# Kernel optimization log

Measured on AMD Instinct MI355X. Metric: run time of the kernel, lower is better.

Reference implementation:

```python
import jax, jax.numpy as jnp
import numpy as np

KS = 7  # transform conv kernel size


def setup_inputs() -> dict:
    key = jax.random.key(0)
    kx, kq, kk, kv, kt = jax.random.split(key, 5)
    b, c, h, w = 4, 64, 64, 64
    x = jax.random.normal(kx, (b, c, h, w), dtype=jnp.float32)
    # 1x1 convs (out_channel=1, bias=False) -> weight vectors over channels
    q_w = jax.random.normal(kq, (c,), dtype=jnp.float32) * 0.05
    k_w = jax.random.normal(kk, (c,), dtype=jnp.float32) * 0.05
    v_w = jax.random.normal(kv, (c,), dtype=jnp.float32) * 0.05
    # transform conv: 1 -> 1 channel, 7x7, reflect pad, no bias
    t_w = jax.random.normal(kt, (1, 1, KS, KS), dtype=jnp.float32) * 0.05
    return {"x": x, "q_w": q_w, "k_w": k_w, "v_w": v_w, "t_w": t_w}


def reference(x, q_w, k_w, v_w, t_w):
    b, c, h, w = x.shape
    hw = h * w
    # 1x1 convs to single channel, flattened over spatial dims -> [b, HW]
    q = jnp.einsum('bchw,c->bhw', x, q_w).reshape(b, hw)
    k = jnp.einsum('bchw,c->bhw', x, k_w).reshape(b, hw)
    v = jnp.einsum('bchw,c->bhw', x, v_w).reshape(b, hw)
    # degenerate head_dim=1 attention: scores are an outer product [b, HW, HW]
    scores = q[:, :, None] * k[:, None, :]
    attn_w = jax.nn.softmax(scores, axis=-1)
    attn = jnp.einsum('bij,bj->bi', attn_w, v).reshape(b, 1, h, w)
    # transform: reflect-pad then 7x7 valid conv
    pad = KS // 2
    attn_p = jnp.pad(attn, ((0, 0), (0, 0), (pad, pad), (pad, pad)), mode='reflect')
    out = jax.lax.conv_general_dilated(
        attn_p, t_w, window_strides=(1, 1), padding='VALID',
        dimension_numbers=('NCHW', 'OIHW', 'NCHW'))
    return out
```

## Files before the change

kernel.cpp:

```cpp
#include <hip/hip_runtime.h>

#define C 64
#define HW 4096
#define NM 20
#define SIG 0x7E3A91D4u
#define PSTRIDE 112
#define PBASE 4096

__device__ __constant__ float INVF[NM] = {
    1.0000000000e+00f, 1.0000000000e+00f, 5.0000000000e-01f, 1.6666666667e-01f,
    4.1666666667e-02f, 8.3333333333e-03f, 1.3888888889e-03f, 1.9841269841e-04f,
    2.4801587302e-05f, 2.7557319224e-06f, 2.7557319224e-07f, 2.5052108385e-08f,
    2.0876756988e-09f, 1.6059043837e-10f, 1.1470745598e-11f, 7.6471637318e-13f,
    4.7794773324e-14f, 2.8114572543e-15f, 1.5619206968e-16f, 8.2206352466e-18f
};

__device__ __forceinline__ void st_rlx(uint32_t* p, uint32_t v) {
    __hip_atomic_store(p, v, __ATOMIC_RELAXED, __HIP_MEMORY_SCOPE_AGENT);
}
__device__ __forceinline__ uint32_t ld_rlx(const uint32_t* p) {
    return __hip_atomic_load(p, __ATOMIC_RELAXED, __HIP_MEMORY_SCOPE_AGENT);
}
__device__ __forceinline__ int reflect64(int r) {
    return r < 0 ? -r : (r > 63 ? 126 - r : r);
}

__global__ __launch_bounds__(256) void fused_kernel(
    const float* __restrict__ x,
    const float* __restrict__ qw,
    const float* __restrict__ kw,
    const float* __restrict__ vw,
    const float* __restrict__ tw,
    float* __restrict__ out,
    uint32_t* __restrict__ W) {
    __shared__ float pq[4][64], pk[4][64], pv[4][64];
    __shared__ float kk[64], vv[64];
    __shared__ float red[64 * 41];
    __shared__ float wred[4][40];
    __shared__ float cf[2 * NM];
    __shared__ float q_lds[7][64];
    __shared__ float attn_s[7][64];
    __shared__ float wgt[49];

    const int tid = threadIdx.x;
    const int p = tid & 63;
    const int wv = tid >> 6;
    const int bl = blockIdx.x;
    const int b = bl >> 6, y = bl & 63;

    uint32_t* flags = W;
    uint32_t* part = W + PBASE + bl * PSTRIDE;

    const float* xb = x + ((size_t)b * C + wv * 16) * HW + y * 64 + p;
    float qa = 0.f, ka = 0.f, va = 0.f;
#pragma unroll
    for (int c = 0; c < 16; ++c) {
        float xv = xb[(size_t)c * HW];
        qa = fmaf(xv, qw[wv * 16 + c], qa);
        ka = fmaf(xv, kw[wv * 16 + c], ka);
        va = fmaf(xv, vw[wv * 16 + c], va);
    }
    pq[wv][p] = qa; pk[wv][p] = ka; pv[wv][p] = va;
    if (tid < 49) wgt[tid] = tw[tid];
    __syncthreads();

    if (wv == 0) {
        float qf = (pq[0][p] + pq[1][p]) + (pq[2][p] + pq[3][p]);
        float kf = (pk[0][p] + pk[1][p]) + (pk[2][p] + pk[3][p]);
        float vf = (pv[0][p] + pv[1][p]) + (pv[2][p] + pv[3][p]);
        st_rlx(part + 40 + p, __float_as_uint(qf));
        kk[p] = kf; vv[p] = vf; q_lds[3][p] = qf;
    }
    __syncthreads();

    {
        float k1 = kk[p], v1 = vv[p];
        float t = 1.f;
        if (wv != 0) {
            float k2 = k1 * k1, k4 = k2 * k2, k5 = k4 * k1;
            t = k5;
            if (wv == 2) t = k5 * k5;
            if (wv == 3) t = (k5 * k5) * k5;
        }
#pragma unroll
        for (int j = 0; j < 5; ++j) {
            red[p * 41 + 5 * wv + j] = t;
            red[p * 41 + 20 + 5 * wv + j] = t * v1;
            t *= k1;
        }
    }
    __syncthreads();

    if (p < 2 * NM) {
        float s = 0.f;
#pragma unroll
        for (int i = 0; i < 16; ++i) s += red[(wv * 16 + i) * 41 + p];
        wred[wv][p] = s;
    }
    __syncthreads();
    if (tid < 2 * NM) {
        float s = (wred[0][tid] + wred[1][tid]) + (wred[2][tid] + wred[3][tid]);
        s *= INVF[tid < NM ? tid : tid - NM];
        st_rlx(part + tid, __float_as_uint(s));
    }
    asm volatile("s_waitcnt vmcnt(0)" ::: "memory");
    __syncthreads();
    if (tid == 0) st_rlx(flags + bl, SIG);

    if (wv == 0) {
        const uint32_t* f = flags + b * 64 + p;
        bool done = false;
        int guard = 0;
        while (true) {
            if (!done) done = (ld_rlx(f) == SIG);
            if (__all(done)) break;
            if (++guard > (1 << 16)) break;
            __builtin_amdgcn_s_sleep(1);
        }
        asm volatile("" ::: "memory");
        if (p < 2 * NM) {
            uint32_t t[64];
            const uint32_t* pb = W + PBASE + (b * 64) * PSTRIDE + p;
#pragma unroll
            for (int s = 0; s < 64; ++s) t[s] = ld_rlx(pb + s * PSTRIDE);
            float fs[64];
#pragma unroll
            for (int s = 0; s < 64; ++s) fs[s] = __uint_as_float(t[s]);
#pragma unroll
            for (int st = 1; st < 64; st <<= 1)
#pragma unroll
                for (int i = 0; i < 64; i += 2 * st) fs[i] += fs[i + st];
            cf[p] = fs[0];
        }
    } else {
        int oA = (wv == 1) ? 0 : (wv == 2) ? 2 : 5;
        int oB = (wv == 1) ? 1 : (wv == 2) ? 4 : 6;
        int rA = reflect64(y + oA - 3);
        int rB = reflect64(y + oB - 3);
        bool needA = (rA != y), needB = (rB != y);
        const uint32_t* fA = flags + b * 64 + rA;
        const uint32_t* fB = flags + b * 64 + rB;
        int guard = 0;
        while (true) {
            bool ok = (!needA || ld_rlx(fA) == SIG) &&
                      (!needB || ld_rlx(fB) == SIG);
            if (ok) break;
            if (++guard > (1 << 16)) break;
            __builtin_amdgcn_s_sleep(1);
        }
        asm volatile("" ::: "memory");
        float hA = needA
            ? __uint_as_float(ld_rlx(W + PBASE + (b * 64 + rA) * PSTRIDE + 40 + p))
            : q_lds[3][p];
        float hB = needB
            ? __uint_as_float(ld_rlx(W + PBASE + (b * 64 + rB) * PSTRIDE + 40 + p))
            : q_lds[3][p];
        q_lds[oA][p] = hA;
        q_lds[oB][p] = hB;
    }
    __syncthreads();

#pragma unroll
    for (int pass = 0; pass < 2; ++pass) {
        int s = pass * 256 + tid;
        int o = s >> 6, cc = s & 63;
        if (o < 7) {
            float qv = q_lds[o][cc];
            float ng = cf[NM - 1], nf = cf[2 * NM - 1];
#pragma unroll
            for (int mm = NM - 2; mm >= 0; --mm) {
                ng = fmaf(ng, qv, cf[mm]);
                nf = fmaf(nf, qv, cf[NM + mm]);
            }
            attn_s[o][cc] = nf / ng;
        }
    }
    __syncthreads();

    if (wv == 0) {
        float acc = 0.f;
#pragma unroll
        for (int dy = 0; dy < 7; ++dy) {
#pragma unroll
            for (int dx = 0; dx < 7; ++dx) {
                int xx = p + dx - 3;
                xx = xx < 0 ? -xx : (xx > 63 ? 126 - xx : xx);
                acc = fmaf(attn_s[dy][xx], wgt[dy * 7 + dx], acc);
            }
        }
        out[(size_t)b * HW + y * 64 + p] = acc;
    }
}

extern "C" void kernel_launch(void* const* d_in, const int* in_sizes, int n_in,
                              void* d_out, int out_size, void* d_ws, size_t ws_size,
                              hipStream_t stream) {
    const float* x  = (const float*)d_in[0];
    const float* qw = (const float*)d_in[1];
    const float* kw = (const float*)d_in[2];
    const float* vw = (const float*)d_in[3];
    const float* tw = (const float*)d_in[4];
    float* out = (float*)d_out;
    uint32_t* W = (uint32_t*)d_ws;

    fused_kernel<<<256, 256, 0, stream>>>(x, qw, kw, vw, tw, out, W);
}
```

Before: 11.82 us.

## Split cross-block coefficient reduction and 7x7 conv across all four waves

```diff
diff --git a/kernel.cpp b/kernel.cpp
--- a/kernel.cpp
+++ b/kernel.cpp
@@ -37,9 +37,11 @@
     __shared__ float kk[64], vv[64];
     __shared__ float red[64 * 41];
     __shared__ float wred[4][40];
+    __shared__ float gred[4][40];
     __shared__ float cf[2 * NM];
     __shared__ float q_lds[7][64];
     __shared__ float attn_s[7][64];
+    __shared__ float cacc[4][64];
     __shared__ float wgt[49];
 
     const int tid = threadIdx.x;
@@ -104,10 +106,9 @@
         st_rlx(part + tid, __float_as_uint(s));
     }
     asm volatile("s_waitcnt vmcnt(0)" ::: "memory");
-    __syncthreads();
     if (tid == 0) st_rlx(flags + bl, SIG);
 
-    if (wv == 0) {
+    {
         const uint32_t* f = flags + b * 64 + p;
         bool done = false;
         int guard = 0;
@@ -118,45 +119,45 @@
             __builtin_amdgcn_s_sleep(1);
         }
         asm volatile("" ::: "memory");
-        if (p < 2 * NM) {
-            uint32_t t[64];
-            const uint32_t* pb = W + PBASE + (b * 64) * PSTRIDE + p;
-#pragma unroll
-            for (int s = 0; s < 64; ++s) t[s] = ld_rlx(pb + s * PSTRIDE);
-            float fs[64];
-#pragma unroll
-            for (int s = 0; s < 64; ++s) fs[s] = __uint_as_float(t[s]);
-#pragma unroll
-            for (int st = 1; st < 64; st <<= 1)
-#pragma unroll
-                for (int i = 0; i < 64; i += 2 * st) fs[i] += fs[i + st];
-            cf[p] = fs[0];
-        }
-    } else {
-        int oA = (wv == 1) ? 0 : (wv == 2) ? 2 : 5;
-        int oB = (wv == 1) ? 1 : (wv == 2) ? 4 : 6;
+    }
+
+    float hA = 0.f, hB = 0.f;
+    int oA = 0, oB = 0;
+    bool needA = false, needB = false;
+    if (wv != 0) {
+        oA = (wv == 1) ? 0 : (wv == 2) ? 2 : 5;
+        oB = (wv == 1) ? 1 : (wv == 2) ? 4 : 6;
         int rA = reflect64(y + oA - 3);
         int rB = reflect64(y + oB - 3);
-        bool needA = (rA != y), needB = (rB != y);
-        const uint32_t* fA = flags + b * 64 + rA;
-        const uint32_t* fB = flags + b * 64 + rB;
-        int guard = 0;
-        while (true) {
-            bool ok = (!needA || ld_rlx(fA) == SIG) &&
-                      (!needB || ld_rlx(fB) == SIG);
-            if (ok) break;
-            if (++guard > (1 << 16)) break;
-            __builtin_amdgcn_s_sleep(1);
-        }
-        asm volatile("" ::: "memory");
-        float hA = needA
-            ? __uint_as_float(ld_rlx(W + PBASE + (b * 64 + rA) * PSTRIDE + 40 + p))
-            : q_lds[3][p];
-        float hB = needB
-            ? __uint_as_float(ld_rlx(W + PBASE + (b * 64 + rB) * PSTRIDE + 40 + p))
-            : q_lds[3][p];
-        q_lds[oA][p] = hA;
-        q_lds[oB][p] = hB;
+        needA = (rA != y); needB = (rB != y);
+        uint32_t uA = needA
+            ? ld_rlx(W + PBASE + (b * 64 + rA) * PSTRIDE + 40 + p) : 0u;
+        uint32_t uB = needB
+            ? ld_rlx(W + PBASE + (b * 64 + rB) * PSTRIDE + 40 + p) : 0u;
+        hA = __uint_as_float(uA);
+        hB = __uint_as_float(uB);
+    }
+    if (p < 2 * NM) {
+        uint32_t t[16];
+        const uint32_t* pb = W + PBASE + (b * 64 + wv * 16) * PSTRIDE + p;
+#pragma unroll
+        for (int s = 0; s < 16; ++s) t[s] = ld_rlx(pb + s * PSTRIDE);
+        float fs[16];
+#pragma unroll
+        for (int s = 0; s < 16; ++s) fs[s] = __uint_as_float(t[s]);
+#pragma unroll
+        for (int st = 1; st < 16; st <<= 1)
+#pragma unroll
+            for (int i = 0; i < 16; i += 2 * st) fs[i] += fs[i + st];
+        gred[wv][p] = fs[0];
+    }
+    if (wv != 0) {
+        if (needA) q_lds[oA][p] = hA; else q_lds[oA][p] = q_lds[3][p];
+        if (needB) q_lds[oB][p] = hB; else q_lds[oB][p] = q_lds[3][p];
+    }
+    __syncthreads();
+    if (tid < 2 * NM) {
+        cf[tid] = (gred[0][tid] + gred[1][tid]) + (gred[2][tid] + gred[3][tid]);
     }
     __syncthreads();
 
@@ -177,17 +178,21 @@
     }
     __syncthreads();
 
+    {
+        float acc = 0.f;
+        int d0 = wv * 2, d1 = (wv < 3) ? wv * 2 + 1 : -1;
+#pragma unroll
+        for (int dx = 0; dx < 7; ++dx) {
+            int xx = p + dx - 3;
+            xx = xx < 0 ? -xx : (xx > 63 ? 126 - xx : xx);
+            acc = fmaf(attn_s[d0][xx], wgt[d0 * 7 + dx], acc);
+            if (d1 >= 0) acc = fmaf(attn_s[d1][xx], wgt[d1 * 7 + dx], acc);
+        }
+        cacc[wv][p] = acc;
+    }
+    __syncthreads();
     if (wv == 0) {
-        float acc = 0.f;
-#pragma unroll
-        for (int dy = 0; dy < 7; ++dy) {
-#pragma unroll
-            for (int dx = 0; dx < 7; ++dx) {
-                int xx = p + dx - 3;
-                xx = xx < 0 ? -xx : (xx > 63 ? 126 - xx : xx);
-                acc = fmaf(attn_s[dy][xx], wgt[dy * 7 + dx], acc);
-            }
-        }
+        float acc = (cacc[0][p] + cacc[1][p]) + (cacc[2][p] + cacc[3][p]);
         out[(size_t)b * HW + y * 64 + p] = acc;
     }
 }
```

Measured after the change: 12.16 us. 1.03x slower.
